# Kernel tuning notes

Hardware: AMD Instinct MI355X
Metric: run time of the kernel (lower is better)

Reference implementation:

```python
import jax, jax.numpy as jnp
import numpy as np

TOP_K = 2  # MoE top-k routing


def setup_inputs() -> dict:
    key = jax.random.key(0)
    ks = jax.random.split(key, 5)
    B, D, H, O, N = 8192, 3072, 128, 10, 8
    scale_g = 1.0 / np.sqrt(D)
    return {
        "x": jax.random.normal(ks[0], (B, D), dtype=jnp.float32),
        "Wg": jax.random.normal(ks[1], (D, N), dtype=jnp.float32) * scale_g,
        "bg": jnp.zeros((N,), dtype=jnp.float32),
        "W1": jax.random.normal(ks[2], (N, D, H), dtype=jnp.float32) * scale_g,
        "b1": jnp.zeros((N, H), dtype=jnp.float32),
        "W2": jax.random.normal(ks[3], (N, H, O), dtype=jnp.float32) * (1.0 / np.sqrt(H)),
        "b2": jnp.zeros((N, O), dtype=jnp.float32),
    }


def reference(x, Wg, bg, W1, b1, W2, b2):
    # Gating: logits -> top-k -> softmax over the k selected logits
    g = x @ Wg + bg                                  # [B, N]
    tv, ti = jax.lax.top_k(g, TOP_K)                 # [B, k]
    w = jax.nn.softmax(tv, axis=-1)                  # [B, k]
    # Expert MLPs, computed densely over all experts (vectorized dispatch)
    h = jax.nn.relu(jnp.einsum('bd,edh->beh', x, W1) + b1)   # [B, N, H]
    y = jnp.einsum('beh,eho->beo', h, W2) + b2               # [B, N, O]
    # Combine: gather each token's k selected expert outputs, weight, sum
    ysel = jnp.take_along_axis(y, ti[:, :, None], axis=1)    # [B, k, O]
    return jnp.sum(w[:, :, None] * ysel, axis=1)             # [B, O]
```

## Files before the change

kernel.cpp:

```cpp
#include <hip/hip_runtime.h>
#include <hip/hip_bf16.h>

#define B_TOK 8192
#define D_DIM 3072
#define H_DIM 128
#define O_DIM 10
#define N_EXP 8

#define BM 128
#define BK2 128
#define HLDS_STRIDE 136
#define CHK 768
#define NCHK 4
#define ESTRIDE 4096

typedef __bf16 bf16x8 __attribute__((ext_vector_type(8)));
typedef float  f32x4  __attribute__((ext_vector_type(4)));
typedef unsigned short us8 __attribute__((ext_vector_type(8)));

__device__ __forceinline__ unsigned short f2bf(float f) {
  unsigned int u = __float_as_uint(f);
  unsigned int r = (u + 0x7FFFu + ((u >> 16) & 1u)) >> 16;
  return (unsigned short)r;
}

__device__ __forceinline__ void async16(const void* g, void* l) {
  __builtin_amdgcn_global_load_lds(
      (const __attribute__((address_space(1))) void*)g,
      (__attribute__((address_space(3))) void*)l,
      16, 0, 0);
}

__global__ __launch_bounds__(256) void k0_w1_transpose(const float* __restrict__ W1,
                                                       unsigned short* __restrict__ w1t) {
  __shared__ __align__(16) unsigned short lds[64 * 72];
  const int e  = blockIdx.z;
  const int d0 = blockIdx.x * 64;
  const int h0 = blockIdx.y * 64;
  const int tid = threadIdx.x;

  const float* src = W1 + ((size_t)e * D_DIM + d0) * H_DIM + h0;
  const int hl = tid & 63;
  const int dg = tid >> 6;
#pragma unroll
  for (int k = 0; k < 16; ++k) {
    const int d = dg + 4 * k;
    lds[hl * 72 + d] = f2bf(src[(size_t)d * H_DIM + hl]);
  }
  __syncthreads();

  unsigned short* dst = w1t + ((size_t)e * H_DIM + h0) * D_DIM + d0;
  const int q  = tid & 7;
  const int h1 = tid >> 3;
#pragma unroll
  for (int k = 0; k < 2; ++k) {
    const int h = h1 + 32 * k;
    const int d = q * 8;
    us8 v = *(const us8*)(lds + h * 72 + d);
    *(us8*)(dst + (size_t)h * D_DIM + d) = v;
  }
}

__global__ __launch_bounds__(256) void k1a_stream(
    const float* __restrict__ x, const float* __restrict__ Wg,
    unsigned short* __restrict__ xb, float* __restrict__ gpart) {
  const int c   = blockIdx.y;
  const int d0  = c * CHK;
  const int tid = threadIdx.x;
  const int lane = tid & 63;
  const int wv   = tid >> 6;
  const int t0   = blockIdx.x * 16 + wv * 4;

  const float* xr0 = x + (size_t)(t0 + 0) * D_DIM + d0;
  const float* xr1 = x + (size_t)(t0 + 1) * D_DIM + d0;
  const float* xr2 = x + (size_t)(t0 + 2) * D_DIM + d0;
  const float* xr3 = x + (size_t)(t0 + 3) * D_DIM + d0;
  unsigned short* xw0 = xb + (size_t)(t0 + 0) * D_DIM + d0;
  unsigned short* xw1 = xb + (size_t)(t0 + 1) * D_DIM + d0;
  unsigned short* xw2 = xb + (size_t)(t0 + 2) * D_DIM + d0;
  unsigned short* xw3 = xb + (size_t)(t0 + 3) * D_DIM + d0;

  float acc[4][N_EXP];
#pragma unroll
  for (int t = 0; t < 4; ++t)
#pragma unroll
    for (int n = 0; n < N_EXP; ++n) acc[t][n] = 0.f;

#pragma unroll
  for (int s = 0; s < CHK / 256; ++s) {
    const int dl = s * 256 + lane * 4;
    float4 xv0 = *(const float4*)(xr0 + dl);
    float4 xv1 = *(const float4*)(xr1 + dl);
    float4 xv2 = *(const float4*)(xr2 + dl);
    float4 xv3 = *(const float4*)(xr3 + dl);
    const float4* wp = (const float4*)(Wg + (size_t)(d0 + dl) * N_EXP);
    float4 wa[4], wb[4];
#pragma unroll
    for (int j = 0; j < 4; ++j) { wa[j] = wp[2 * j]; wb[j] = wp[2 * j + 1]; }

    ushort4 p;
    p.x = f2bf(xv0.x); p.y = f2bf(xv0.y); p.z = f2bf(xv0.z); p.w = f2bf(xv0.w);
    *(ushort4*)(xw0 + dl) = p;
    p.x = f2bf(xv1.x); p.y = f2bf(xv1.y); p.z = f2bf(xv1.z); p.w = f2bf(xv1.w);
    *(ushort4*)(xw1 + dl) = p;
    p.x = f2bf(xv2.x); p.y = f2bf(xv2.y); p.z = f2bf(xv2.z); p.w = f2bf(xv2.w);
    *(ushort4*)(xw2 + dl) = p;
    p.x = f2bf(xv3.x); p.y = f2bf(xv3.y); p.z = f2bf(xv3.z); p.w = f2bf(xv3.w);
    *(ushort4*)(xw3 + dl) = p;

    float xe0[4] = {xv0.x, xv0.y, xv0.z, xv0.w};
    float xe1[4] = {xv1.x, xv1.y, xv1.z, xv1.w};
    float xe2[4] = {xv2.x, xv2.y, xv2.z, xv2.w};
    float xe3[4] = {xv3.x, xv3.y, xv3.z, xv3.w};
#pragma unroll
    for (int j = 0; j < 4; ++j) {
      acc[0][0] = fmaf(xe0[j], wa[j].x, acc[0][0]);
      acc[0][1] = fmaf(xe0[j], wa[j].y, acc[0][1]);
      acc[0][2] = fmaf(xe0[j], wa[j].z, acc[0][2]);
      acc[0][3] = fmaf(xe0[j], wa[j].w, acc[0][3]);
      acc[0][4] = fmaf(xe0[j], wb[j].x, acc[0][4]);
      acc[0][5] = fmaf(xe0[j], wb[j].y, acc[0][5]);
      acc[0][6] = fmaf(xe0[j], wb[j].z, acc[0][6]);
      acc[0][7] = fmaf(xe0[j], wb[j].w, acc[0][7]);
      acc[1][0] = fmaf(xe1[j], wa[j].x, acc[1][0]);
      acc[1][1] = fmaf(xe1[j], wa[j].y, acc[1][1]);
      acc[1][2] = fmaf(xe1[j], wa[j].z, acc[1][2]);
      acc[1][3] = fmaf(xe1[j], wa[j].w, acc[1][3]);
      acc[1][4] = fmaf(xe1[j], wb[j].x, acc[1][4]);
      acc[1][5] = fmaf(xe1[j], wb[j].y, acc[1][5]);
      acc[1][6] = fmaf(xe1[j], wb[j].z, acc[1][6]);
      acc[1][7] = fmaf(xe1[j], wb[j].w, acc[1][7]);
      acc[2][0] = fmaf(xe2[j], wa[j].x, acc[2][0]);
      acc[2][1] = fmaf(xe2[j], wa[j].y, acc[2][1]);
      acc[2][2] = fmaf(xe2[j], wa[j].z, acc[2][2]);
      acc[2][3] = fmaf(xe2[j], wa[j].w, acc[2][3]);
      acc[2][4] = fmaf(xe2[j], wb[j].x, acc[2][4]);
      acc[2][5] = fmaf(xe2[j], wb[j].y, acc[2][5]);
      acc[2][6] = fmaf(xe2[j], wb[j].z, acc[2][6]);
      acc[2][7] = fmaf(xe2[j], wb[j].w, acc[2][7]);
      acc[3][0] = fmaf(xe3[j], wa[j].x, acc[3][0]);
      acc[3][1] = fmaf(xe3[j], wa[j].y, acc[3][1]);
      acc[3][2] = fmaf(xe3[j], wa[j].z, acc[3][2]);
      acc[3][3] = fmaf(xe3[j], wa[j].w, acc[3][3]);
      acc[3][4] = fmaf(xe3[j], wb[j].x, acc[3][4]);
      acc[3][5] = fmaf(xe3[j], wb[j].y, acc[3][5]);
      acc[3][6] = fmaf(xe3[j], wb[j].z, acc[3][6]);
      acc[3][7] = fmaf(xe3[j], wb[j].w, acc[3][7]);
    }
  }

#pragma unroll
  for (int t = 0; t < 4; ++t)
#pragma unroll
    for (int n = 0; n < N_EXP; ++n) {
#pragma unroll
      for (int off = 32; off > 0; off >>= 1)
        acc[t][n] += __shfl_xor(acc[t][n], off, 64);
    }
  if (lane == 0) {
#pragma unroll
    for (int t = 0; t < 4; ++t) {
      float* gp = gpart + ((size_t)c * B_TOK + (t0 + t)) * N_EXP;
      *(float4*)(gp)     = make_float4(acc[t][0], acc[t][1], acc[t][2], acc[t][3]);
      *(float4*)(gp + 4) = make_float4(acc[t][4], acc[t][5], acc[t][6], acc[t][7]);
    }
  }
}

__global__ __launch_bounds__(256) void k1c_topk(
    const float* __restrict__ gpart, const float* __restrict__ bg,
    int4* __restrict__ idx4, float2* __restrict__ wts, int* __restrict__ cnt,
    int* __restrict__ tlist) {
  __shared__ int lcnt[N_EXP], gbase[N_EXP];
  __shared__ float bgs[N_EXP];
  const int tid = threadIdx.x;
  if (tid < N_EXP) { lcnt[tid] = 0; bgs[tid] = bg[tid]; }
  __syncthreads();
  const int t = blockIdx.x * 256 + tid;

  float g[N_EXP];
#pragma unroll
  for (int n = 0; n < N_EXP; ++n) g[n] = bgs[n];
#pragma unroll
  for (int c = 0; c < NCHK; ++c) {
    const float* gp = gpart + ((size_t)c * B_TOK + t) * N_EXP;
    float4 a = *(const float4*)(gp);
    float4 b = *(const float4*)(gp + 4);
    g[0] += a.x; g[1] += a.y; g[2] += a.z; g[3] += a.w;
    g[4] += b.x; g[5] += b.y; g[6] += b.z; g[7] += b.w;
  }
  int i0 = 0;
#pragma unroll
  for (int n = 1; n < N_EXP; ++n) if (g[n] > g[i0]) i0 = n;
  int i1 = (i0 == 0) ? 1 : 0;
#pragma unroll
  for (int n = 0; n < N_EXP; ++n) if (n != i0 && g[n] > g[i1]) i1 = n;
  const float e1 = expf(g[i1] - g[i0]);
  const float inv = 1.f / (1.f + e1);
  const int lp0 = atomicAdd(&lcnt[i0], 1);
  const int lp1 = atomicAdd(&lcnt[i1], 1);
  __syncthreads();
  if (tid < N_EXP) gbase[tid] = atomicAdd(&cnt[tid], lcnt[tid]);
  __syncthreads();
  int p0 = gbase[i0] + lp0; p0 = p0 < ESTRIDE ? p0 : ESTRIDE - 1;
  int p1 = gbase[i1] + lp1; p1 = p1 < ESTRIDE ? p1 : ESTRIDE - 1;
  tlist[i0 * ESTRIDE + p0] = t;
  tlist[i1 * ESTRIDE + p1] = t;
  idx4[t] = make_int4(i0, p0, i1, p1);
  wts[t]  = make_float2(inv, e1 * inv);
}

__global__ __launch_bounds__(256) void k2_experts(
    const unsigned short* __restrict__ xb,
    const unsigned short* __restrict__ w1t,
    const float* __restrict__ b1,
    const float* __restrict__ W2,
    const float* __restrict__ b2,
    const int* __restrict__ cnt, const int* __restrict__ tlist,
    float* __restrict__ ypair) {
  const int e    = blockIdx.y;
  int n_e        = cnt[e];
  n_e            = n_e < ESTRIDE ? n_e : ESTRIDE;
  const int row0 = blockIdx.x * BM;
  if (row0 >= n_e) return;

  __shared__ __align__(16) unsigned short sm[65536 + 2048];
  unsigned short* h_lds   = sm;
  unsigned short* w2t_lds = sm + 65536;

  const int tid  = threadIdx.x;
  const int lane = tid & 63;
  const int wv   = tid >> 6;
  const int quad = lane >> 4;
  const int cl   = lane & 15;

  const unsigned short* Abase[8];
  const unsigned short* Bbase[8];
#pragma unroll
  for (int j = 0; j < 8; ++j) {
    const int rloc = wv * 32 + j * 4 + quad;
    int gr = row0 + rloc;
    gr = gr < n_e ? gr : n_e - 1;
    const int koff = ((cl - (j * 4 + quad)) & 15) * 8;
    Abase[j] = xb + (size_t)tlist[e * ESTRIDE + gr] * D_DIM + koff;
    Bbase[j] = w1t + ((size_t)e * H_DIM + rloc) * D_DIM + koff;
  }

#define STAGE(it, pp)                                                     \
  {                                                                       \
    const int ko = (it) * BK2;                                            \
    unsigned short* abuf = sm + (pp) * 32768;                             \
    unsigned short* bbuf = sm + 16384 + (pp) * 32768;                     \
    _Pragma("unroll")                                                     \
    for (int j = 0; j < 8; ++j) {                                         \
      const int ldsrow = (wv * 32 + j * 4) * BK2;                         \
      async16(Abase[j] + ko, abuf + ldsrow);                              \
      async16(Bbase[j] + ko, bbuf + ldsrow);                              \
    }                                                                     \
  }

  STAGE(0, 0);

  const float* W2e = W2 + (size_t)e * H_DIM * O_DIM;
  for (int idx = tid; idx < 16 * 128; idx += 256) {
    const int o = idx >> 7, hh = idx & 127;
    const float v = (o < O_DIM) ? W2e[hh * O_DIM + o] : 0.f;
    w2t_lds[o * 128 + ((((hh >> 3) + o) & 15) * 8) + (hh & 7)] = f2bf(v);
  }

  const int mhalf = (wv >> 1) * 64;
  const int nhalf = (wv & 1) * 64;

  f32x4 acc[4][4];
#pragma unroll
  for (int i = 0; i < 4; ++i)
#pragma unroll
    for (int j = 0; j < 4; ++j)
      acc[i][j] = (f32x4){0.f, 0.f, 0.f, 0.f};

  const int NIT = D_DIM / BK2;
  for (int it = 0; it < NIT; ++it) {
    __syncthreads();
    if (it + 1 < NIT) STAGE(it + 1, (it + 1) & 1);
    const unsigned short* al = sm + (it & 1) * 32768;
    const unsigned short* bl = sm + 16384 + (it & 1) * 32768;
#pragma unroll
    for (int kk = 0; kk < 4; ++kk) {
      const int pos = ((kk * 4 + quad + cl) & 15) * 8;
      bf16x8 af[4], bfr[4];
#pragma unroll
      for (int mi = 0; mi < 4; ++mi)
        af[mi] = *(const bf16x8*)(al + (mhalf + mi * 16 + cl) * BK2 + pos);
#pragma unroll
      for (int ni = 0; ni < 4; ++ni)
        bfr[ni] = *(const bf16x8*)(bl + (nhalf + ni * 16 + cl) * BK2 + pos);
#pragma unroll
      for (int mi = 0; mi < 4; ++mi)
#pragma unroll
        for (int ni = 0; ni < 4; ++ni)
          acc[mi][ni] = __builtin_amdgcn_mfma_f32_16x16x32_bf16(af[mi], bfr[ni], acc[mi][ni], 0, 0, 0);
    }
  }
  __syncthreads();

  const float* b1e = b1 + e * H_DIM;
#pragma unroll
  for (int ni = 0; ni < 4; ++ni) {
    const int col  = nhalf + ni * 16 + cl;
    const float bias = b1e[col];
#pragma unroll
    for (int mi = 0; mi < 4; ++mi) {
      const int rbase = mhalf + mi * 16 + (quad << 2);
#pragma unroll
      for (int r = 0; r < 4; ++r) {
        float v = acc[mi][ni][r] + bias;
        v = v > 0.f ? v : 0.f;
        h_lds[(rbase + r) * HLDS_STRIDE + col] = f2bf(v);
      }
    }
  }
  __syncthreads();

  f32x4 acc2[2];
  acc2[0] = (f32x4){0.f, 0.f, 0.f, 0.f};
  acc2[1] = (f32x4){0.f, 0.f, 0.f, 0.f};
#pragma unroll
  for (int ks = 0; ks < 4; ++ks) {
    const int krd = ks * 32 + quad * 8;
    bf16x8 bfr = *(const bf16x8*)(w2t_lds + cl * 128 + ((ks * 4 + quad + cl) & 15) * 8);
#pragma unroll
    for (int mi = 0; mi < 2; ++mi) {
      bf16x8 afr = *(const bf16x8*)(h_lds + (wv * 32 + mi * 16 + cl) * HLDS_STRIDE + krd);
      acc2[mi] = __builtin_amdgcn_mfma_f32_16x16x32_bf16(afr, bfr, acc2[mi], 0, 0, 0);
    }
  }
  const int o = cl;
  if (o < O_DIM) {
    const float bias2 = b2[e * O_DIM + o];
#pragma unroll
    for (int mi = 0; mi < 2; ++mi) {
#pragma unroll
      for (int r = 0; r < 4; ++r) {
        const int rl = wv * 32 + mi * 16 + (quad << 2) + r;
        if (row0 + rl < n_e)
          ypair[(size_t)(e * ESTRIDE + row0 + rl) * 16 + o] = acc2[mi][r] + bias2;
      }
    }
  }
}

__global__ __launch_bounds__(256) void k3_combine(
    const float* __restrict__ ypair, const int4* __restrict__ idx4,
    const float2* __restrict__ wts, float* __restrict__ out) {
  const int g = blockIdx.x * 256 + threadIdx.x;
  if (g >= B_TOK * O_DIM) return;
  const int b = g / O_DIM, o = g - b * O_DIM;
  const int4 r = idx4[b];
  const float2 w = wts[b];
  out[g] = w.x * ypair[(size_t)(r.x * ESTRIDE + r.y) * 16 + o] +
           w.y * ypair[(size_t)(r.z * ESTRIDE + r.w) * 16 + o];
}

extern "C" void kernel_launch(void* const* d_in, const int* in_sizes, int n_in,
                              void* d_out, int out_size, void* d_ws, size_t ws_size,
                              hipStream_t stream) {
  const float* x  = (const float*)d_in[0];
  const float* Wg = (const float*)d_in[1];
  const float* bg = (const float*)d_in[2];
  const float* W1 = (const float*)d_in[3];
  const float* b1 = (const float*)d_in[4];
  const float* W2 = (const float*)d_in[5];
  const float* b2 = (const float*)d_in[6];
  float* out = (float*)d_out;

  char* ws = (char*)d_ws;
  unsigned short* xb  = (unsigned short*)ws;
  unsigned short* w1t = (unsigned short*)(ws + 50331648);
  int4*   idx4  = (int4*)  (ws + 56623104);
  float2* wts   = (float2*)(ws + 56754176);
  int*    cnt   = (int*)   (ws + 56819712);
  int*    tlist = (int*)   (ws + 56819840);
  float*  gpart = (float*) (ws + 56950912);
  float*  ypair = (float*) (ws + 56950912);

  k0_w1_transpose<<<dim3(48, 2, 8), dim3(256), 0, stream>>>(W1, w1t);
  (void)hipMemsetAsync(cnt, 0, N_EXP * sizeof(int), stream);
  k1a_stream<<<dim3(B_TOK / 16, NCHK), dim3(256), 0, stream>>>(x, Wg, xb, gpart);
  k1c_topk<<<dim3(B_TOK / 256), dim3(256), 0, stream>>>(gpart, bg, idx4, wts, cnt, tlist);
  k2_experts<<<dim3(ESTRIDE / BM, N_EXP), dim3(256), 0, stream>>>(
      xb, w1t, b1, W2, b2, cnt, tlist, ypair);
  k3_combine<<<dim3((B_TOK * O_DIM + 255) / 256), dim3(256), 0, stream>>>(
      ypair, idx4, wts, out);
}
```

Before: 237.4 us.

## Fuse gate GEMV and top-k routing into one kernel over full D

The gating stream kernel now processes the full D dimension per block instead of splitting into 4 chunks, so the partial-logit buffer and the separate top-k kernel are removed. Top-k, softmax weights and expert slot assignment are computed directly in the gate kernel by lanes 0-3 of each wave. Loads are batched four float4 steps at a time to raise memory-level parallelism. This removes one launch and the gpart round trip, but the grid shrinks from 2048 to 512 blocks, and per-block global atomics on cnt rise from 32 to 512 blocks.

```diff
diff --git a/kernel.cpp b/kernel.cpp
--- a/kernel.cpp
+++ b/kernel.cpp
@@ -10,8 +10,6 @@
 #define BM 128
 #define BK2 128
 #define HLDS_STRIDE 136
-#define CHK 768
-#define NCHK 4
 #define ESTRIDE 4096
 
 typedef __bf16 bf16x8 __attribute__((ext_vector_type(8)));
@@ -61,24 +59,29 @@
   }
 }
 
-__global__ __launch_bounds__(256) void k1a_stream(
+__global__ __launch_bounds__(256) void k1_gate(
     const float* __restrict__ x, const float* __restrict__ Wg,
-    unsigned short* __restrict__ xb, float* __restrict__ gpart) {
-  const int c   = blockIdx.y;
-  const int d0  = c * CHK;
-  const int tid = threadIdx.x;
+    const float* __restrict__ bg,
+    unsigned short* __restrict__ xb,
+    int4* __restrict__ idx4, float2* __restrict__ wts,
+    int* __restrict__ cnt, int* __restrict__ tlist) {
+  __shared__ int lcnt[N_EXP], gbase[N_EXP];
+  const int tid  = threadIdx.x;
+  if (tid < N_EXP) lcnt[tid] = 0;
+  __syncthreads();
+
   const int lane = tid & 63;
   const int wv   = tid >> 6;
   const int t0   = blockIdx.x * 16 + wv * 4;
 
-  const float* xr0 = x + (size_t)(t0 + 0) * D_DIM + d0;
-  const float* xr1 = x + (size_t)(t0 + 1) * D_DIM + d0;
-  const float* xr2 = x + (size_t)(t0 + 2) * D_DIM + d0;
-  const float* xr3 = x + (size_t)(t0 + 3) * D_DIM + d0;
-  unsigned short* xw0 = xb + (size_t)(t0 + 0) * D_DIM + d0;
-  unsigned short* xw1 = xb + (size_t)(t0 + 1) * D_DIM + d0;
-  unsigned short* xw2 = xb + (size_t)(t0 + 2) * D_DIM + d0;
-  unsigned short* xw3 = xb + (size_t)(t0 + 3) * D_DIM + d0;
+  const float* xr0 = x + (size_t)(t0 + 0) * D_DIM;
+  const float* xr1 = x + (size_t)(t0 + 1) * D_DIM;
+  const float* xr2 = x + (size_t)(t0 + 2) * D_DIM;
+  const float* xr3 = x + (size_t)(t0 + 3) * D_DIM;
+  unsigned short* xw0 = xb + (size_t)(t0 + 0) * D_DIM;
+  unsigned short* xw1 = xb + (size_t)(t0 + 1) * D_DIM;
+  unsigned short* xw2 = xb + (size_t)(t0 + 2) * D_DIM;
+  unsigned short* xw3 = xb + (size_t)(t0 + 3) * D_DIM;
 
   float acc[4][N_EXP];
 #pragma unroll
@@ -86,66 +89,73 @@
 #pragma unroll
     for (int n = 0; n < N_EXP; ++n) acc[t][n] = 0.f;
 
-#pragma unroll
-  for (int s = 0; s < CHK / 256; ++s) {
-    const int dl = s * 256 + lane * 4;
-    float4 xv0 = *(const float4*)(xr0 + dl);
-    float4 xv1 = *(const float4*)(xr1 + dl);
-    float4 xv2 = *(const float4*)(xr2 + dl);
-    float4 xv3 = *(const float4*)(xr3 + dl);
-    const float4* wp = (const float4*)(Wg + (size_t)(d0 + dl) * N_EXP);
-    float4 wa[4], wb[4];
-#pragma unroll
-    for (int j = 0; j < 4; ++j) { wa[j] = wp[2 * j]; wb[j] = wp[2 * j + 1]; }
-
-    ushort4 p;
-    p.x = f2bf(xv0.x); p.y = f2bf(xv0.y); p.z = f2bf(xv0.z); p.w = f2bf(xv0.w);
-    *(ushort4*)(xw0 + dl) = p;
-    p.x = f2bf(xv1.x); p.y = f2bf(xv1.y); p.z = f2bf(xv1.z); p.w = f2bf(xv1.w);
-    *(ushort4*)(xw1 + dl) = p;
-    p.x = f2bf(xv2.x); p.y = f2bf(xv2.y); p.z = f2bf(xv2.z); p.w = f2bf(xv2.w);
-    *(ushort4*)(xw2 + dl) = p;
-    p.x = f2bf(xv3.x); p.y = f2bf(xv3.y); p.z = f2bf(xv3.z); p.w = f2bf(xv3.w);
-    *(ushort4*)(xw3 + dl) = p;
-
-    float xe0[4] = {xv0.x, xv0.y, xv0.z, xv0.w};
-    float xe1[4] = {xv1.x, xv1.y, xv1.z, xv1.w};
-    float xe2[4] = {xv2.x, xv2.y, xv2.z, xv2.w};
-    float xe3[4] = {xv3.x, xv3.y, xv3.z, xv3.w};
-#pragma unroll
-    for (int j = 0; j < 4; ++j) {
-      acc[0][0] = fmaf(xe0[j], wa[j].x, acc[0][0]);
-      acc[0][1] = fmaf(xe0[j], wa[j].y, acc[0][1]);
-      acc[0][2] = fmaf(xe0[j], wa[j].z, acc[0][2]);
-      acc[0][3] = fmaf(xe0[j], wa[j].w, acc[0][3]);
-      acc[0][4] = fmaf(xe0[j], wb[j].x, acc[0][4]);
-      acc[0][5] = fmaf(xe0[j], wb[j].y, acc[0][5]);
-      acc[0][6] = fmaf(xe0[j], wb[j].z, acc[0][6]);
-      acc[0][7] = fmaf(xe0[j], wb[j].w, acc[0][7]);
-      acc[1][0] = fmaf(xe1[j], wa[j].x, acc[1][0]);
-      acc[1][1] = fmaf(xe1[j], wa[j].y, acc[1][1]);
-      acc[1][2] = fmaf(xe1[j], wa[j].z, acc[1][2]);
-      acc[1][3] = fmaf(xe1[j], wa[j].w, acc[1][3]);
-      acc[1][4] = fmaf(xe1[j], wb[j].x, acc[1][4]);
-      acc[1][5] = fmaf(xe1[j], wb[j].y, acc[1][5]);
-      acc[1][6] = fmaf(xe1[j], wb[j].z, acc[1][6]);
-      acc[1][7] = fmaf(xe1[j], wb[j].w, acc[1][7]);
-      acc[2][0] = fmaf(xe2[j], wa[j].x, acc[2][0]);
-      acc[2][1] = fmaf(xe2[j], wa[j].y, acc[2][1]);
-      acc[2][2] = fmaf(xe2[j], wa[j].z, acc[2][2]);
-      acc[2][3] = fmaf(xe2[j], wa[j].w, acc[2][3]);
-      acc[2][4] = fmaf(xe2[j], wb[j].x, acc[2][4]);
-      acc[2][5] = fmaf(xe2[j], wb[j].y, acc[2][5]);
-      acc[2][6] = fmaf(xe2[j], wb[j].z, acc[2][6]);
-      acc[2][7] = fmaf(xe2[j], wb[j].w, acc[2][7]);
-      acc[3][0] = fmaf(xe3[j], wa[j].x, acc[3][0]);
-      acc[3][1] = fmaf(xe3[j], wa[j].y, acc[3][1]);
-      acc[3][2] = fmaf(xe3[j], wa[j].z, acc[3][2]);
-      acc[3][3] = fmaf(xe3[j], wa[j].w, acc[3][3]);
-      acc[3][4] = fmaf(xe3[j], wb[j].x, acc[3][4]);
-      acc[3][5] = fmaf(xe3[j], wb[j].y, acc[3][5]);
-      acc[3][6] = fmaf(xe3[j], wb[j].z, acc[3][6]);
-      acc[3][7] = fmaf(xe3[j], wb[j].w, acc[3][7]);
+  for (int grp = 0; grp < 3; ++grp) {
+    float4 xv0[4], xv1[4], xv2[4], xv3[4];
+#pragma unroll
+    for (int s = 0; s < 4; ++s) {
+      const int dl = (grp * 4 + s) * 256 + lane * 4;
+      xv0[s] = *(const float4*)(xr0 + dl);
+      xv1[s] = *(const float4*)(xr1 + dl);
+      xv2[s] = *(const float4*)(xr2 + dl);
+      xv3[s] = *(const float4*)(xr3 + dl);
+    }
+#pragma unroll
+    for (int s = 0; s < 4; ++s) {
+      const int dl = (grp * 4 + s) * 256 + lane * 4;
+      const float4* wp = (const float4*)(Wg + (size_t)dl * N_EXP);
+      float4 wa[4], wb[4];
+#pragma unroll
+      for (int j = 0; j < 4; ++j) { wa[j] = wp[2 * j]; wb[j] = wp[2 * j + 1]; }
+
+      ushort4 p;
+      p.x = f2bf(xv0[s].x); p.y = f2bf(xv0[s].y); p.z = f2bf(xv0[s].z); p.w = f2bf(xv0[s].w);
+      *(ushort4*)(xw0 + dl) = p;
+      p.x = f2bf(xv1[s].x); p.y = f2bf(xv1[s].y); p.z = f2bf(xv1[s].z); p.w = f2bf(xv1[s].w);
+      *(ushort4*)(xw1 + dl) = p;
+      p.x = f2bf(xv2[s].x); p.y = f2bf(xv2[s].y); p.z = f2bf(xv2[s].z); p.w = f2bf(xv2[s].w);
+      *(ushort4*)(xw2 + dl) = p;
+      p.x = f2bf(xv3[s].x); p.y = f2bf(xv3[s].y); p.z = f2bf(xv3[s].z); p.w = f2bf(xv3[s].w);
+      *(ushort4*)(xw3 + dl) = p;
+
+      float xe0[4] = {xv0[s].x, xv0[s].y, xv0[s].z, xv0[s].w};
+      float xe1[4] = {xv1[s].x, xv1[s].y, xv1[s].z, xv1[s].w};
+      float xe2[4] = {xv2[s].x, xv2[s].y, xv2[s].z, xv2[s].w};
+      float xe3[4] = {xv3[s].x, xv3[s].y, xv3[s].z, xv3[s].w};
+#pragma unroll
+      for (int j = 0; j < 4; ++j) {
+        acc[0][0] = fmaf(xe0[j], wa[j].x, acc[0][0]);
+        acc[0][1] = fmaf(xe0[j], wa[j].y, acc[0][1]);
+        acc[0][2] = fmaf(xe0[j], wa[j].z, acc[0][2]);
+        acc[0][3] = fmaf(xe0[j], wa[j].w, acc[0][3]);
+        acc[0][4] = fmaf(xe0[j], wb[j].x, acc[0][4]);
+        acc[0][5] = fmaf(xe0[j], wb[j].y, acc[0][5]);
+        acc[0][6] = fmaf(xe0[j], wb[j].z, acc[0][6]);
+        acc[0][7] = fmaf(xe0[j], wb[j].w, acc[0][7]);
+        acc[1][0] = fmaf(xe1[j], wa[j].x, acc[1][0]);
+        acc[1][1] = fmaf(xe1[j], wa[j].y, acc[1][1]);
+        acc[1][2] = fmaf(xe1[j], wa[j].z, acc[1][2]);
+        acc[1][3] = fmaf(xe1[j], wa[j].w, acc[1][3]);
+        acc[1][4] = fmaf(xe1[j], wb[j].x, acc[1][4]);
+        acc[1][5] = fmaf(xe1[j], wb[j].y, acc[1][5]);
+        acc[1][6] = fmaf(xe1[j], wb[j].z, acc[1][6]);
+        acc[1][7] = fmaf(xe1[j], wb[j].w, acc[1][7]);
+        acc[2][0] = fmaf(xe2[j], wa[j].x, acc[2][0]);
+        acc[2][1] = fmaf(xe2[j], wa[j].y, acc[2][1]);
+        acc[2][2] = fmaf(xe2[j], wa[j].z, acc[2][2]);
+        acc[2][3] = fmaf(xe2[j], wa[j].w, acc[2][3]);
+        acc[2][4] = fmaf(xe2[j], wb[j].x, acc[2][4]);
+        acc[2][5] = fmaf(xe2[j], wb[j].y, acc[2][5]);
+        acc[2][6] = fmaf(xe2[j], wb[j].z, acc[2][6]);
+        acc[2][7] = fmaf(xe2[j], wb[j].w, acc[2][7]);
+        acc[3][0] = fmaf(xe3[j], wa[j].x, acc[3][0]);
+        acc[3][1] = fmaf(xe3[j], wa[j].y, acc[3][1]);
+        acc[3][2] = fmaf(xe3[j], wa[j].z, acc[3][2]);
+        acc[3][3] = fmaf(xe3[j], wa[j].w, acc[3][3]);
+        acc[3][4] = fmaf(xe3[j], wb[j].x, acc[3][4]);
+        acc[3][5] = fmaf(xe3[j], wb[j].y, acc[3][5]);
+        acc[3][6] = fmaf(xe3[j], wb[j].z, acc[3][6]);
+        acc[3][7] = fmaf(xe3[j], wb[j].w, acc[3][7]);
+      }
     }
   }
 
@@ -157,57 +167,45 @@
       for (int off = 32; off > 0; off >>= 1)
         acc[t][n] += __shfl_xor(acc[t][n], off, 64);
     }
-  if (lane == 0) {
-#pragma unroll
-    for (int t = 0; t < 4; ++t) {
-      float* gp = gpart + ((size_t)c * B_TOK + (t0 + t)) * N_EXP;
-      *(float4*)(gp)     = make_float4(acc[t][0], acc[t][1], acc[t][2], acc[t][3]);
-      *(float4*)(gp + 4) = make_float4(acc[t][4], acc[t][5], acc[t][6], acc[t][7]);
-    }
-  }
-}
-
-__global__ __launch_bounds__(256) void k1c_topk(
-    const float* __restrict__ gpart, const float* __restrict__ bg,
-    int4* __restrict__ idx4, float2* __restrict__ wts, int* __restrict__ cnt,
-    int* __restrict__ tlist) {
-  __shared__ int lcnt[N_EXP], gbase[N_EXP];
-  __shared__ float bgs[N_EXP];
-  const int tid = threadIdx.x;
-  if (tid < N_EXP) { lcnt[tid] = 0; bgs[tid] = bg[tid]; }
-  __syncthreads();
-  const int t = blockIdx.x * 256 + tid;
-
-  float g[N_EXP];
-#pragma unroll
-  for (int n = 0; n < N_EXP; ++n) g[n] = bgs[n];
-#pragma unroll
-  for (int c = 0; c < NCHK; ++c) {
-    const float* gp = gpart + ((size_t)c * B_TOK + t) * N_EXP;
-    float4 a = *(const float4*)(gp);
-    float4 b = *(const float4*)(gp + 4);
-    g[0] += a.x; g[1] += a.y; g[2] += a.z; g[3] += a.w;
-    g[4] += b.x; g[5] += b.y; g[6] += b.z; g[7] += b.w;
-  }
-  int i0 = 0;
-#pragma unroll
-  for (int n = 1; n < N_EXP; ++n) if (g[n] > g[i0]) i0 = n;
-  int i1 = (i0 == 0) ? 1 : 0;
-#pragma unroll
-  for (int n = 0; n < N_EXP; ++n) if (n != i0 && g[n] > g[i1]) i1 = n;
-  const float e1 = expf(g[i1] - g[i0]);
-  const float inv = 1.f / (1.f + e1);
-  const int lp0 = atomicAdd(&lcnt[i0], 1);
-  const int lp1 = atomicAdd(&lcnt[i1], 1);
+
+  int i0 = 0, i1 = 0, lp0 = 0, lp1 = 0;
+  float w0 = 0.f, w1 = 0.f;
+  if (lane < 4) {
+    float g[N_EXP];
+#pragma unroll
+    for (int n = 0; n < N_EXP; ++n) {
+      float v = acc[0][n];
+      v = (lane == 1) ? acc[1][n] : v;
+      v = (lane == 2) ? acc[2][n] : v;
+      v = (lane == 3) ? acc[3][n] : v;
+      g[n] = v + bg[n];
+    }
+    float m0 = g[0];
+#pragma unroll
+    for (int n = 1; n < N_EXP; ++n)
+      if (g[n] > m0) { m0 = g[n]; i0 = n; }
+    float m1 = -3.4e38f;
+#pragma unroll
+    for (int n = 0; n < N_EXP; ++n)
+      if (n != i0 && g[n] > m1) { m1 = g[n]; i1 = n; }
+    const float e1  = expf(m1 - m0);
+    const float inv = 1.f / (1.f + e1);
+    w0 = inv; w1 = e1 * inv;
+    lp0 = atomicAdd(&lcnt[i0], 1);
+    lp1 = atomicAdd(&lcnt[i1], 1);
+  }
   __syncthreads();
   if (tid < N_EXP) gbase[tid] = atomicAdd(&cnt[tid], lcnt[tid]);
   __syncthreads();
-  int p0 = gbase[i0] + lp0; p0 = p0 < ESTRIDE ? p0 : ESTRIDE - 1;
-  int p1 = gbase[i1] + lp1; p1 = p1 < ESTRIDE ? p1 : ESTRIDE - 1;
-  tlist[i0 * ESTRIDE + p0] = t;
-  tlist[i1 * ESTRIDE + p1] = t;
-  idx4[t] = make_int4(i0, p0, i1, p1);
-  wts[t]  = make_float2(inv, e1 * inv);
+  if (lane < 4) {
+    const int t = t0 + lane;
+    int p0 = gbase[i0] + lp0; p0 = p0 < ESTRIDE ? p0 : ESTRIDE - 1;
+    int p1 = gbase[i1] + lp1; p1 = p1 < ESTRIDE ? p1 : ESTRIDE - 1;
+    tlist[i0 * ESTRIDE + p0] = t;
+    tlist[i1 * ESTRIDE + p1] = t;
+    idx4[t] = make_int4(i0, p0, i1, p1);
+    wts[t]  = make_float2(w0, w1);
+  }
 }
 
 __global__ __launch_bounds__(256) void k2_experts(
@@ -380,13 +378,12 @@
   float2* wts   = (float2*)(ws + 56754176);
   int*    cnt   = (int*)   (ws + 56819712);
   int*    tlist = (int*)   (ws + 56819840);
-  float*  gpart = (float*) (ws + 56950912);
   float*  ypair = (float*) (ws + 56950912);
 
   k0_w1_transpose<<<dim3(48, 2, 8), dim3(256), 0, stream>>>(W1, w1t);
   (void)hipMemsetAsync(cnt, 0, N_EXP * sizeof(int), stream);
-  k1a_stream<<<dim3(B_TOK / 16, NCHK), dim3(256), 0, stream>>>(x, Wg, xb, gpart);
-  k1c_topk<<<dim3(B_TOK / 256), dim3(256), 0, stream>>>(gpart, bg, idx4, wts, cnt, tlist);
+  k1_gate<<<dim3(B_TOK / 16), dim3(256), 0, stream>>>(
+      x, Wg, bg, xb, idx4, wts, cnt, tlist);
   k2_experts<<<dim3(ESTRIDE / BM, N_EXP), dim3(256), 0, stream>>>(
       xb, w1t, b1, W2, b2, cnt, tlist, ypair);
   k3_combine<<<dim3((B_TOK * O_DIM + 255) / 256), dim3(256), 0, stream>>>(
```

New measurement: 244.5 us. 3.0% more time.

## Fuse combine into expert kernel via atomic adds and halve expert row tile

Applied to the files above, without the earlier changes.

Removes the separate combine kernel. Each expert block now multiplies its outputs by the routing weight, stored per slot by the top-k kernel, and atomically adds them into the zeroed output. The expert GEMM row tile drops from 128 to 64, which doubles the block count and cuts LDS use for better occupancy. The cost is that W1 tiles are reloaded twice as often, and fp32 atomic accumulation makes the order of summation nondeterministic.

```diff
diff --git a/kernel.cpp b/kernel.cpp
--- a/kernel.cpp
+++ b/kernel.cpp
@@ -7,7 +7,7 @@
 #define O_DIM 10
 #define N_EXP 8
 
-#define BM 128
+#define BM 64
 #define BK2 128
 #define HLDS_STRIDE 136
 #define CHK 768
@@ -169,8 +169,7 @@
 
 __global__ __launch_bounds__(256) void k1c_topk(
     const float* __restrict__ gpart, const float* __restrict__ bg,
-    int4* __restrict__ idx4, float2* __restrict__ wts, int* __restrict__ cnt,
-    int* __restrict__ tlist) {
+    int* __restrict__ cnt, int* __restrict__ tlist, float* __restrict__ wslot) {
   __shared__ int lcnt[N_EXP], gbase[N_EXP];
   __shared__ float bgs[N_EXP];
   const int tid = threadIdx.x;
@@ -206,8 +205,8 @@
   int p1 = gbase[i1] + lp1; p1 = p1 < ESTRIDE ? p1 : ESTRIDE - 1;
   tlist[i0 * ESTRIDE + p0] = t;
   tlist[i1 * ESTRIDE + p1] = t;
-  idx4[t] = make_int4(i0, p0, i1, p1);
-  wts[t]  = make_float2(inv, e1 * inv);
+  wslot[i0 * ESTRIDE + p0] = inv;
+  wslot[i1 * ESTRIDE + p1] = e1 * inv;
 }
 
 __global__ __launch_bounds__(256) void k2_experts(
@@ -217,16 +216,17 @@
     const float* __restrict__ W2,
     const float* __restrict__ b2,
     const int* __restrict__ cnt, const int* __restrict__ tlist,
-    float* __restrict__ ypair) {
+    const float* __restrict__ wslot,
+    float* __restrict__ out) {
   const int e    = blockIdx.y;
   int n_e        = cnt[e];
   n_e            = n_e < ESTRIDE ? n_e : ESTRIDE;
   const int row0 = blockIdx.x * BM;
   if (row0 >= n_e) return;
 
-  __shared__ __align__(16) unsigned short sm[65536 + 2048];
+  __shared__ __align__(16) unsigned short sm[49152 + 2048];
   unsigned short* h_lds   = sm;
-  unsigned short* w2t_lds = sm + 65536;
+  unsigned short* w2t_lds = sm + 49152;
 
   const int tid  = threadIdx.x;
   const int lane = tid & 63;
@@ -234,29 +234,34 @@
   const int quad = lane >> 4;
   const int cl   = lane & 15;
 
-  const unsigned short* Abase[8];
+  const unsigned short* Abase[4];
   const unsigned short* Bbase[8];
 #pragma unroll
-  for (int j = 0; j < 8; ++j) {
-    const int rloc = wv * 32 + j * 4 + quad;
+  for (int j = 0; j < 4; ++j) {
+    const int rloc = wv * 16 + j * 4 + quad;
     int gr = row0 + rloc;
     gr = gr < n_e ? gr : n_e - 1;
     const int koff = ((cl - (j * 4 + quad)) & 15) * 8;
     Abase[j] = xb + (size_t)tlist[e * ESTRIDE + gr] * D_DIM + koff;
+  }
+#pragma unroll
+  for (int j = 0; j < 8; ++j) {
+    const int rloc = wv * 32 + j * 4 + quad;
+    const int koff = ((cl - (j * 4 + quad)) & 15) * 8;
     Bbase[j] = w1t + ((size_t)e * H_DIM + rloc) * D_DIM + koff;
   }
 
 #define STAGE(it, pp)                                                     \
   {                                                                       \
     const int ko = (it) * BK2;                                            \
-    unsigned short* abuf = sm + (pp) * 32768;                             \
-    unsigned short* bbuf = sm + 16384 + (pp) * 32768;                     \
+    unsigned short* abuf = sm + (pp) * 24576;                             \
+    unsigned short* bbuf = sm + 8192 + (pp) * 24576;                      \
     _Pragma("unroll")                                                     \
-    for (int j = 0; j < 8; ++j) {                                         \
-      const int ldsrow = (wv * 32 + j * 4) * BK2;                         \
-      async16(Abase[j] + ko, abuf + ldsrow);                              \
-      async16(Bbase[j] + ko, bbuf + ldsrow);                              \
-    }                                                                     \
+    for (int j = 0; j < 4; ++j)                                           \
+      async16(Abase[j] + ko, abuf + (wv * 16 + j * 4) * BK2);             \
+    _Pragma("unroll")                                                     \
+    for (int j = 0; j < 8; ++j)                                           \
+      async16(Bbase[j] + ko, bbuf + (wv * 32 + j * 4) * BK2);             \
   }
 
   STAGE(0, 0);
@@ -268,12 +273,12 @@
     w2t_lds[o * 128 + ((((hh >> 3) + o) & 15) * 8) + (hh & 7)] = f2bf(v);
   }
 
-  const int mhalf = (wv >> 1) * 64;
-  const int nhalf = (wv & 1) * 64;
-
-  f32x4 acc[4][4];
-#pragma unroll
-  for (int i = 0; i < 4; ++i)
+  const int mhalf = (wv & 1) * 32;
+  const int nhalf = (wv >> 1) * 64;
+
+  f32x4 acc[2][4];
+#pragma unroll
+  for (int i = 0; i < 2; ++i)
 #pragma unroll
     for (int j = 0; j < 4; ++j)
       acc[i][j] = (f32x4){0.f, 0.f, 0.f, 0.f};
@@ -282,20 +287,20 @@
   for (int it = 0; it < NIT; ++it) {
     __syncthreads();
     if (it + 1 < NIT) STAGE(it + 1, (it + 1) & 1);
-    const unsigned short* al = sm + (it & 1) * 32768;
-    const unsigned short* bl = sm + 16384 + (it & 1) * 32768;
+    const unsigned short* al = sm + (it & 1) * 24576;
+    const unsigned short* bl = sm + 8192 + (it & 1) * 24576;
 #pragma unroll
     for (int kk = 0; kk < 4; ++kk) {
       const int pos = ((kk * 4 + quad + cl) & 15) * 8;
-      bf16x8 af[4], bfr[4];
-#pragma unroll
-      for (int mi = 0; mi < 4; ++mi)
+      bf16x8 af[2], bfr[4];
+#pragma unroll
+      for (int mi = 0; mi < 2; ++mi)
         af[mi] = *(const bf16x8*)(al + (mhalf + mi * 16 + cl) * BK2 + pos);
 #pragma unroll
       for (int ni = 0; ni < 4; ++ni)
         bfr[ni] = *(const bf16x8*)(bl + (nhalf + ni * 16 + cl) * BK2 + pos);
 #pragma unroll
-      for (int mi = 0; mi < 4; ++mi)
+      for (int mi = 0; mi < 2; ++mi)
 #pragma unroll
         for (int ni = 0; ni < 4; ++ni)
           acc[mi][ni] = __builtin_amdgcn_mfma_f32_16x16x32_bf16(af[mi], bfr[ni], acc[mi][ni], 0, 0, 0);
@@ -309,7 +314,7 @@
     const int col  = nhalf + ni * 16 + cl;
     const float bias = b1e[col];
 #pragma unroll
-    for (int mi = 0; mi < 4; ++mi) {
+    for (int mi = 0; mi < 2; ++mi) {
       const int rbase = mhalf + mi * 16 + (quad << 2);
 #pragma unroll
       for (int r = 0; r < 4; ++r) {
@@ -321,44 +326,28 @@
   }
   __syncthreads();
 
-  f32x4 acc2[2];
-  acc2[0] = (f32x4){0.f, 0.f, 0.f, 0.f};
-  acc2[1] = (f32x4){0.f, 0.f, 0.f, 0.f};
+  f32x4 acc2 = (f32x4){0.f, 0.f, 0.f, 0.f};
 #pragma unroll
   for (int ks = 0; ks < 4; ++ks) {
     const int krd = ks * 32 + quad * 8;
     bf16x8 bfr = *(const bf16x8*)(w2t_lds + cl * 128 + ((ks * 4 + quad + cl) & 15) * 8);
-#pragma unroll
-    for (int mi = 0; mi < 2; ++mi) {
-      bf16x8 afr = *(const bf16x8*)(h_lds + (wv * 32 + mi * 16 + cl) * HLDS_STRIDE + krd);
-      acc2[mi] = __builtin_amdgcn_mfma_f32_16x16x32_bf16(afr, bfr, acc2[mi], 0, 0, 0);
-    }
+    bf16x8 afr = *(const bf16x8*)(h_lds + (wv * 16 + cl) * HLDS_STRIDE + krd);
+    acc2 = __builtin_amdgcn_mfma_f32_16x16x32_bf16(afr, bfr, acc2, 0, 0, 0);
   }
   const int o = cl;
   if (o < O_DIM) {
     const float bias2 = b2[e * O_DIM + o];
 #pragma unroll
-    for (int mi = 0; mi < 2; ++mi) {
-#pragma unroll
-      for (int r = 0; r < 4; ++r) {
-        const int rl = wv * 32 + mi * 16 + (quad << 2) + r;
-        if (row0 + rl < n_e)
-          ypair[(size_t)(e * ESTRIDE + row0 + rl) * 16 + o] = acc2[mi][r] + bias2;
+    for (int r = 0; r < 4; ++r) {
+      const int rl = wv * 16 + (quad << 2) + r;
+      const int slot = row0 + rl;
+      if (slot < n_e) {
+        const int t = tlist[e * ESTRIDE + slot];
+        const float w = wslot[e * ESTRIDE + slot];
+        atomicAdd(out + (size_t)t * O_DIM + o, w * (acc2[r] + bias2));
       }
     }
   }
-}
-
-__global__ __launch_bounds__(256) void k3_combine(
-    const float* __restrict__ ypair, const int4* __restrict__ idx4,
-    const float2* __restrict__ wts, float* __restrict__ out) {
-  const int g = blockIdx.x * 256 + threadIdx.x;
-  if (g >= B_TOK * O_DIM) return;
-  const int b = g / O_DIM, o = g - b * O_DIM;
-  const int4 r = idx4[b];
-  const float2 w = wts[b];
-  out[g] = w.x * ypair[(size_t)(r.x * ESTRIDE + r.y) * 16 + o] +
-           w.y * ypair[(size_t)(r.z * ESTRIDE + r.w) * 16 + o];
 }
 
 extern "C" void kernel_launch(void* const* d_in, const int* in_sizes, int n_in,
@@ -376,19 +365,16 @@
   char* ws = (char*)d_ws;
   unsigned short* xb  = (unsigned short*)ws;
   unsigned short* w1t = (unsigned short*)(ws + 50331648);
-  int4*   idx4  = (int4*)  (ws + 56623104);
-  float2* wts   = (float2*)(ws + 56754176);
-  int*    cnt   = (int*)   (ws + 56819712);
-  int*    tlist = (int*)   (ws + 56819840);
-  float*  gpart = (float*) (ws + 56950912);
-  float*  ypair = (float*) (ws + 56950912);
+  int*    cnt   = (int*)   (ws + 56623104);
+  int*    tlist = (int*)   (ws + 56623232);
+  float*  wslot = (float*) (ws + 56754304);
+  float*  gpart = (float*) (ws + 56885376);
 
   k0_w1_transpose<<<dim3(48, 2, 8), dim3(256), 0, stream>>>(W1, w1t);
   (void)hipMemsetAsync(cnt, 0, N_EXP * sizeof(int), stream);
+  (void)hipMemsetAsync(out, 0, (size_t)B_TOK * O_DIM * sizeof(float), stream);
   k1a_stream<<<dim3(B_TOK / 16, NCHK), dim3(256), 0, stream>>>(x, Wg, xb, gpart);
-  k1c_topk<<<dim3(B_TOK / 256), dim3(256), 0, stream>>>(gpart, bg, idx4, wts, cnt, tlist);
+  k1c_topk<<<dim3(B_TOK / 256), dim3(256), 0, stream>>>(gpart, bg, cnt, tlist, wslot);
   k2_experts<<<dim3(ESTRIDE / BM, N_EXP), dim3(256), 0, stream>>>(
-      xb, w1t, b1, W2, b2, cnt, tlist, ypair);
-  k3_combine<<<dim3((B_TOK * O_DIM + 255) / 256), dim3(256), 0, stream>>>(
-      ypair, idx4, wts, out);
-}
+      xb, w1t, b1, W2, b2, cnt, tlist, wslot, out);
+}
```

New measurement: 246.3 us. 1.04x slower.
